# Performance work log

Measured on AMD Instinct MI355X. Metric: run time of the kernel, lower is better.

## Reference

```python
import jax, jax.numpy as jnp
import numpy as np

B, S, D, H, V = 4, 2048, 128, 4, 64
HD = D // H
ITERS = 3
SCALE = 1.0 / float(np.sqrt(HD))
APO = 0.2
TRP = 0.15
FC = 1.61803
EPS = 1e-5


def ln(x, g, b):
    m = x.mean(-1, keepdims=True)
    v = ((x - m) ** 2).mean(-1, keepdims=True)
    return (x - m) / jnp.sqrt(v + EPS) * g + b


def setup_inputs() -> dict:
    key = jax.random.key(0)
    ks = iter(jax.random.split(key, 64))

    def w(shape, s=0.02):
        return jax.random.normal(next(ks), shape, jnp.float32) * s

    return {
        "x": jax.random.normal(next(ks), (B, S, D), jnp.float32),
        "space": jax.random.normal(next(ks), (B, S, D), jnp.float32),
        # attn_norm
        "g_attn": jnp.ones(D), "b_attn": jnp.zeros(D),
        # RecursiveScaledDotProductAttention
        "Wq": w((D, D)), "Wk": w((D, D)), "Wv": w((D, D)),
        "Wo": w((D, D)), "bo": jnp.zeros(D),
        "Wg": w((D, 2 * D)), "bg": jnp.zeros(D),
        "Wobs": w((H, D)), "bobs": jnp.zeros(H),
        # trp_norm + TraumaResolutionPathLayer
        "g_trp": jnp.ones(D), "b_trp": jnp.zeros(D),
        "Wt": w((V, D)), "bt": jnp.zeros(V),
        "Wc": w((V, D)), "bc": jnp.zeros(V),
        "Ws": w((V, D)), "bs": jnp.zeros(V),
        "Wr": w((V, 3 * V)), "br": jnp.zeros(V),
        "fv": jnp.ones(V) * FC,
        "Wop": w((D, V)), "bop": jnp.zeros(D),
        # MorphogenesisFFN
        "g_ffn": jnp.ones(D), "b_ffn": jnp.zeros(D),
        "W1": w((4 * D, D)), "b1": jnp.zeros(4 * D),
        "W2": w((D, 4 * D)), "b2": jnp.zeros(D),
        "Wsg": w((D, D)), "bsg": jnp.zeros(D),
        # ApophasisLayer
        "g_apo": jnp.ones(D), "b_apo": jnp.zeros(D),
        "Wn": w((D, D)), "bn": jnp.zeros(D),
    }


def reference(x, space, g_attn, b_attn, Wq, Wk, Wv, Wo, bo, Wg, bg, Wobs, bobs,
              g_trp, b_trp, Wt, bt, Wc, bc, Ws, bs, Wr, br, fv, Wop, bop,
              g_ffn, b_ffn, W1, b1, W2, b2, Wsg, bsg, g_apo, b_apo, Wn, bn):
    # --- recursive attention (autopoiesis loop, eval mode: dropout = identity) ---
    xn = ln(x, g_attn, b_attn)
    obs = xn.mean(1, keepdims=True)                      # [B,1,D] observer_state default
    infl = (obs @ Wobs.T + bobs).transpose(0, 2, 1)[..., None]  # [B,H,1,1] per-head bias
    cur = xn
    for _ in range(ITERS):
        q = (cur @ Wq.T).reshape(B, S, H, HD).transpose(0, 2, 1, 3)
        k = (cur @ Wk.T).reshape(B, S, H, HD).transpose(0, 2, 1, 3)
        v = (cur @ Wv.T).reshape(B, S, H, HD).transpose(0, 2, 1, 3)
        scores = jnp.einsum('bhqd,bhkd->bhqk', q, k) * SCALE + infl
        aw = jax.nn.softmax(scores, axis=-1)             # [B,H,S,S]
        ao = jnp.einsum('bhqk,bhkd->bhqd', aw, v).transpose(0, 2, 1, 3).reshape(B, S, D)
        out = ao @ Wo.T + bo
        gate = jax.nn.sigmoid(jnp.concatenate([cur, out], -1) @ Wg.T + bg)
        cur = cur * (1 - gate) + out * gate
    x = x + cur
    # --- Trauma Resolution Path ---
    xn2 = ln(x, g_trp, b_trp)
    tv = xn2 @ Wt.T + bt                                 # [B,S,V]
    cv = jnp.broadcast_to(xn2.mean(1, keepdims=True) @ Wc.T + bc, tv.shape)
    sv = space @ Ws.T + bs
    rgate = jax.nn.sigmoid(jnp.concatenate([tv, cv, sv], -1) @ Wr.T + br)
    cn = jnp.maximum(jnp.linalg.norm(cv, axis=-1, keepdims=True), 1e-8)
    sn = jnp.maximum(jnp.linalg.norm(sv, axis=-1, keepdims=True), 1e-8)
    align = (cv * sv).sum(-1, keepdims=True) / (cn * sn)
    resolved = tv + TRP * (-align * (fv - tv) * rgate)
    x = x + resolved @ Wop.T + bop
    # --- Morphogenesis FFN ---
    xn3 = ln(x, g_ffn, b_ffn)
    ff = jax.nn.gelu(xn3 @ W1.T + b1, approximate=False) @ W2.T + b2
    x = x + jax.nn.sigmoid(xn3 @ Wsg.T + bsg) * ff
    # --- Apophasis ---
    x = x - APO * jnp.tanh(ln(x, g_apo, b_apo) @ Wn.T + bn)
    return x, aw
```

## Files before the change

### kernel.cpp

```cpp
#include <hip/hip_runtime.h>
#include <cstdint>
#include <cstddef>


typedef unsigned short u16;
typedef __attribute__((ext_vector_type(8))) short short8;
typedef __attribute__((ext_vector_type(4))) float f32x4;
typedef __attribute__((ext_vector_type(2))) unsigned uint32x2;

#define B_ 4
#define S_ 2048
#define D_ 128
#define H_ 4
#define M_ 8192
#define SCALE2_ 0.25503472510324417f
#define APO_ 0.2f
#define TRP_ 0.15f
#define EPS_ 1e-5f

__device__ __forceinline__ float fexp2(float x){ return __builtin_amdgcn_exp2f(x); }

__device__ __forceinline__ u16 f2bf(float f){
  unsigned u = __float_as_uint(f);
  unsigned r = ((u >> 16) & 1u) + 0x7fffu;
  return (u16)((u + r) >> 16);
}
__device__ __forceinline__ float bf2f(u16 u){ return __uint_as_float(((unsigned)u) << 16); }
__device__ __forceinline__ float sigm(float x){ return 1.0f/(1.0f + __expf(-x)); }

__device__ __forceinline__ unsigned cvtpk_bf16(float lo, float hi){
  unsigned r;
  asm("v_cvt_pk_bf16_f32 %0, %1, %2" : "=v"(r) : "v"(lo), "v"(hi));
  return r;
}

#define LDS_BARRIER() __asm__ volatile("s_waitcnt lgkmcnt(0)\n\ts_barrier" ::: "memory")

struct WSrc { const float* s[13]; };
__global__ __launch_bounds__(256) void prep_k(WSrc w, u16* __restrict__ dst,
    const float* __restrict__ x_in, const float* __restrict__ g,
    const float* __restrict__ b, u16* __restrict__ cg0){
  if (blockIdx.x < 1168){
    int idx = blockIdx.x*256 + threadIdx.x;
    if (idx >= 299008) return;
    const int sz[13] = {16384,16384,16384,16384,32768,8192,8192,12288,8192,65536,65536,16384,16384};
    int off = idx;
    #pragma unroll
    for (int seg = 0; seg < 13; ++seg){
      if (off < sz[seg]) { dst[idx] = f2bf(w.s[seg][off]); return; }
      off -= sz[seg];
    }
  } else {
    int wv = threadIdx.x >> 6, lane = threadIdx.x & 63;
    int row = (blockIdx.x - 1168)*4 + wv;
    size_t rb = (size_t)row * D_;
    float v0 = x_in[rb + lane], v1 = x_in[rb + lane + 64];
    float s = v0 + v1;
    #pragma unroll
    for (int m = 1; m < 64; m <<= 1) s += __shfl_xor(s, m, 64);
    float mean = s * (1.0f/128.0f);
    float d0 = v0 - mean, d1 = v1 - mean;
    float vv = d0*d0 + d1*d1;
    #pragma unroll
    for (int m = 1; m < 64; m <<= 1) vv += __shfl_xor(vv, m, 64);
    float rstd = rsqrtf(vv * (1.0f/128.0f) + EPS_);
    cg0[rb + lane]      = f2bf(d0*rstd*g[lane]    + b[lane]);
    cg0[rb + lane + 64] = f2bf(d1*rstd*g[lane+64] + b[lane+64]);
  }
}

__global__ __launch_bounds__(512) void colmean_k(const u16* __restrict__ lnb,
    const float* __restrict__ Wc, const float* __restrict__ bc,
    float* __restrict__ cv, float* __restrict__ cn){
  __shared__ float red2[32][128];
  __shared__ float cmS[128];
  int b = blockIdx.x;
  int tid = threadIdx.x;
  int rg = tid >> 4, c8 = (tid & 15)*8;
  const u16* pp = lnb + (size_t)b*S_*D_ + (size_t)rg*D_ + c8;
  float acc[8];
  #pragma unroll
  for (int j = 0; j < 8; ++j) acc[j] = 0.f;
  #pragma unroll 4
  for (int i = 0; i < 64; ++i){
    short8 v = *(const short8*)(pp + (size_t)i*32*D_);
    #pragma unroll
    for (int j = 0; j < 8; ++j) acc[j] += bf2f((u16)v[j]);
  }
  #pragma unroll
  for (int j = 0; j < 8; ++j) red2[rg][c8 + j] = acc[j];
  __syncthreads();
  if (tid < 128){
    float s = 0.f;
    #pragma unroll
    for (int r = 0; r < 32; ++r) s += red2[r][tid];
    cmS[tid] = s * (1.0f/2048.0f);
  }
  __syncthreads();
  if (tid < 64){
    int n = tid;
    const float* wrow = Wc + n*D_;
    float sacc = bc[n];
    #pragma unroll 4
    for (int dd = 0; dd < D_; ++dd) sacc += cmS[dd]*wrow[dd];
    cv[b*64 + n] = sacc;
    float sq = sacc*sacc;
    #pragma unroll
    for (int m = 1; m < 64; m <<= 1) sq += __shfl_xor(sq, m, 64);
    if (n == 0) cn[b] = fmaxf(sqrtf(sq), 1e-8f);
  }
}

__global__ __launch_bounds__(256) void gemm_qkv(const u16* __restrict__ A,
    const u16* __restrict__ W, u16* __restrict__ qh, u16* __restrict__ kh, u16* __restrict__ vt){
  __shared__ u16 Asm[64*136];
  __shared__ u16 Bsm[64*136];
  const int m0 = blockIdx.x*64, n0 = blockIdx.y*64;
  int tid = threadIdx.x;
  int wv = tid >> 6, lane = tid & 63, quad = lane >> 4, l15 = lane & 15;
  int wm = wv >> 1, wn = wv & 1;
  {
    int sr = tid >> 2, cb = (tid & 3)*32;
    const u16* ag = A + (size_t)(m0 + sr)*128 + cb;
    const u16* bg = W + (size_t)(n0 + sr)*128 + cb;
    short8 a0 = *(const short8*)(ag + 0);
    short8 a1 = *(const short8*)(ag + 8);
    short8 a2 = *(const short8*)(ag + 16);
    short8 a3 = *(const short8*)(ag + 24);
    short8 b0 = *(const short8*)(bg + 0);
    short8 b1 = *(const short8*)(bg + 8);
    short8 b2 = *(const short8*)(bg + 16);
    short8 b3 = *(const short8*)(bg + 24);
    *(short8*)(Asm + sr*136 + cb + 0)  = a0;
    *(short8*)(Asm + sr*136 + cb + 8)  = a1;
    *(short8*)(Asm + sr*136 + cb + 16) = a2;
    *(short8*)(Asm + sr*136 + cb + 24) = a3;
    *(short8*)(Bsm + sr*136 + cb + 0)  = b0;
    *(short8*)(Bsm + sr*136 + cb + 8)  = b1;
    *(short8*)(Bsm + sr*136 + cb + 16) = b2;
    *(short8*)(Bsm + sr*136 + cb + 24) = b3;
  }
  LDS_BARRIER();
  f32x4 acc[2][2];
  #pragma unroll
  for (int i = 0; i < 2; ++i)
    #pragma unroll
    for (int j = 0; j < 2; ++j) acc[i][j] = (f32x4){0.f,0.f,0.f,0.f};
  #pragma unroll
  for (int k0 = 0; k0 < 128; k0 += 32){
    short8 af0 = *(const short8*)(Asm + (wm*32      + l15)*136 + k0 + quad*8);
    short8 af1 = *(const short8*)(Asm + (wm*32 + 16 + l15)*136 + k0 + quad*8);
    short8 bf0 = *(const short8*)(Bsm + (wn*32      + l15)*136 + k0 + quad*8);
    short8 bf1 = *(const short8*)(Bsm + (wn*32 + 16 + l15)*136 + k0 + quad*8);
    acc[0][0] = __builtin_amdgcn_mfma_f32_16x16x32_bf16(af0, bf0, acc[0][0], 0,0,0);
    acc[0][1] = __builtin_amdgcn_mfma_f32_16x16x32_bf16(af0, bf1, acc[0][1], 0,0,0);
    acc[1][0] = __builtin_amdgcn_mfma_f32_16x16x32_bf16(af1, bf0, acc[1][0], 0,0,0);
    acc[1][1] = __builtin_amdgcn_mfma_f32_16x16x32_bf16(af1, bf1, acc[1][1], 0,0,0);
  }
  #pragma unroll
  for (int ms = 0; ms < 2; ++ms)
    #pragma unroll
    for (int ns = 0; ns < 2; ++ns){
      int mb = m0 + wm*32 + ms*16 + quad*4;
      int nn = n0 + wn*32 + ns*16 + l15;
      int which = nn >> 7, col = nn & 127, h = col >> 5, hd = col & 31;
      f32x4 c = acc[ms][ns];
      #pragma unroll
      for (int r = 0; r < 4; ++r){
        int m = mb + r, b = m >> 11, s = m & 2047;
        if (which == 0)      qh[((size_t)(b*H_+h)*S_ + s)*32 + hd] = f2bf(c[r]);
        else if (which == 1) kh[((size_t)(b*H_+h)*S_ + s)*32 + hd] = f2bf(c[r]);
        else                 vt[((size_t)(b*H_+h)*32 + hd)*S_ + s] = f2bf(c[r]);
      }
    }
}

template<bool WRITE_AW>
__global__ __launch_bounds__(256) void attn_k(const u16* __restrict__ qh, const u16* __restrict__ kh,
    const u16* __restrict__ vT, u16* __restrict__ ao_bf, float* __restrict__ aw){
  __shared__ u16 Ks[2][128*40];
  __shared__ u16 Vs[2][32*136];
  __shared__ u16 Ps[4*16*136];
  int L = blockIdx.y*32 + blockIdx.x;
  int xcd = L & 7, j = L >> 3;
  int bh = 2*xcd + (j >> 5);
  int q0 = (j & 31)*64;
  int b = bh >> 2, h = bh & 3;
  int tid = threadIdx.x, wv = tid >> 6, lane = tid & 63, quad = lane >> 4, l15 = lane & 15;
  int qrow = q0 + wv*16 + l15;
  const size_t bhS = (size_t)bh * S_;
  short8 qf = *(const short8*)(qh + (bhS + qrow)*32 + quad*8);
  int krow = tid >> 1, kseg = (tid & 1)*16;
  const u16* kg = kh + (bhS + krow)*32 + kseg;
  int vrow = tid >> 3, vseg = (tid & 7)*16;
  const u16* vg = vT + ((size_t)bh*32 + vrow)*S_ + vseg;
  f32x4 zero = {0.f,0.f,0.f,0.f};
  f32x4 ao0 = zero, ao1 = zero;
  float lsum = 0.f, rinv = 1.0f, nls = 0.f;
  u16* PsW = Ps + wv*16*136;

  if constexpr (WRITE_AW){
    {
      short8 a0 = *(const short8*)(kg + 0);
      short8 a1 = *(const short8*)(kg + 8);
      *(short8*)(Ks[0] + krow*40 + kseg    ) = a0;
      *(short8*)(Ks[0] + krow*40 + kseg + 8) = a1;
    }
    #pragma unroll 2
    for (int t = 0; t < 16; ++t){
      LDS_BARRIER();
      short8 n0, n1;
      if (t < 15){
        n0 = *(const short8*)(kg + (size_t)(t+1)*4096 + 0);
        n1 = *(const short8*)(kg + (size_t)(t+1)*4096 + 8);
      }
      const u16* Kb = Ks[t & 1];
      #pragma unroll
      for (int jt = 0; jt < 8; ++jt){
        short8 kf = *(const short8*)(Kb + (jt*16 + l15)*40 + quad*8);
        f32x4 s = __builtin_amdgcn_mfma_f32_16x16x32_bf16(kf, qf, zero, 0,0,0);
        #pragma unroll
        for (int r = 0; r < 4; ++r) lsum += fexp2(s[r]*SCALE2_);
      }
      if (t < 15){
        u16* Kn = Ks[(t+1) & 1];
        *(short8*)(Kn + krow*40 + kseg    ) = n0;
        *(short8*)(Kn + krow*40 + kseg + 8) = n1;
      }
    }
    lsum += __shfl_xor(lsum, 16, 64);
    lsum += __shfl_xor(lsum, 32, 64);
    nls = -__log2f(lsum);
  }

  {
    short8 a0 = *(const short8*)(kg + 0);
    short8 a1 = *(const short8*)(kg + 8);
    short8 b0 = *(const short8*)(vg + 0);
    short8 b1 = *(const short8*)(vg + 8);
    *(short8*)(Ks[0] + krow*40 + kseg    ) = a0;
    *(short8*)(Ks[0] + krow*40 + kseg + 8) = a1;
    *(short8*)(Vs[0] + vrow*136 + vseg    ) = b0;
    *(short8*)(Vs[0] + vrow*136 + vseg + 8) = b1;
  }
  #pragma unroll 2
  for (int t = 0; t < 16; ++t){
    LDS_BARRIER();
    short8 kn0, kn1, vn0, vn1;
    if (t < 15){
      kn0 = *(const short8*)(kg + (size_t)(t+1)*4096 + 0);
      kn1 = *(const short8*)(kg + (size_t)(t+1)*4096 + 8);
      vn0 = *(const short8*)(vg + (size_t)(t+1)*128 + 0);
      vn1 = *(const short8*)(vg + (size_t)(t+1)*128 + 8);
    }
    const u16* Kb = Ks[t & 1];
    const u16* Vb = Vs[t & 1];
    int k0 = t*128;
    #pragma unroll
    for (int jt = 0; jt < 8; ++jt){
      short8 kf = *(const short8*)(Kb + (jt*16 + l15)*40 + quad*8);
      f32x4 s = __builtin_amdgcn_mfma_f32_16x16x32_bf16(kf, qf, zero, 0,0,0);
      float pv[4];
      #pragma unroll
      for (int r = 0; r < 4; ++r){
        float e;
        if constexpr (WRITE_AW) e = fexp2(__builtin_fmaf(s[r], SCALE2_, nls));
        else { e = fexp2(s[r]*SCALE2_); lsum += e; }
        pv[r] = e;
      }
      if constexpr (WRITE_AW){
        f32x4 st = {pv[0], pv[1], pv[2], pv[3]};
        *(f32x4*)(aw + (bhS + qrow)*S_ + k0 + jt*16 + quad*4) = st;
      }
      uint32x2 pk;
      pk[0] = cvtpk_bf16(pv[0], pv[1]);
      pk[1] = cvtpk_bf16(pv[2], pv[3]);
      *(uint32x2*)(PsW + l15*136 + jt*16 + quad*4) = pk;
    }
    __asm__ volatile("s_waitcnt lgkmcnt(0)" ::: "memory");
    #pragma unroll
    for (int jg = 0; jg < 4; ++jg){
      short8 pf  = *(const short8*)(PsW + l15*136 + jg*32 + quad*8);
      short8 vf0 = *(const short8*)(Vb + (l15     )*136 + jg*32 + quad*8);
      short8 vf1 = *(const short8*)(Vb + (16 + l15)*136 + jg*32 + quad*8);
      ao0 = __builtin_amdgcn_mfma_f32_16x16x32_bf16(vf0, pf, ao0, 0,0,0);
      ao1 = __builtin_amdgcn_mfma_f32_16x16x32_bf16(vf1, pf, ao1, 0,0,0);
    }
    if (t < 15){
      u16* Kn = Ks[(t+1) & 1];
      u16* Vn = Vs[(t+1) & 1];
      *(short8*)(Kn + krow*40 + kseg    ) = kn0;
      *(short8*)(Kn + krow*40 + kseg + 8) = kn1;
      *(short8*)(Vn + vrow*136 + vseg    ) = vn0;
      *(short8*)(Vn + vrow*136 + vseg + 8) = vn1;
    }
  }

  if constexpr (!WRITE_AW){
    lsum += __shfl_xor(lsum, 16, 64);
    lsum += __shfl_xor(lsum, 32, 64);
    rinv = 1.0f / lsum;
  }

  size_t rowbase = ((size_t)(b*S_ + qrow))*D_ + h*32;
  #pragma unroll
  for (int dt = 0; dt < 2; ++dt){
    f32x4 a = dt ? ao1 : ao0;
    uint32x2 pk;
    pk[0] = cvtpk_bf16(a[0]*rinv, a[1]*rinv);
    pk[1] = cvtpk_bf16(a[2]*rinv, a[3]*rinv);
    *(uint32x2*)(ao_bf + rowbase + dt*16 + quad*4) = pk;
  }
}

template<bool DO_QKV>
__global__ __launch_bounds__(256) void wqkv_k(const u16* __restrict__ cin,
    const u16* __restrict__ ao_bf, const u16* __restrict__ wo, const u16* __restrict__ wg,
    const u16* __restrict__ w3, const float* __restrict__ bo, const float* __restrict__ bg,
    u16* __restrict__ cout, u16* __restrict__ qh, u16* __restrict__ kh, u16* __restrict__ vt,
    const float* __restrict__ x_in, const float* __restrict__ g_trp,
    const float* __restrict__ b_trp, float* __restrict__ xbuf, u16* __restrict__ lnb){
  __shared__ u16 aoS[16*136];
  __shared__ u16 cuS[16*136];
  __shared__ u16 outS[16*136];
  __shared__ u16 coS[16*136];
  const int m0 = blockIdx.x*16;
  int tid = threadIdx.x, wv = tid >> 6, lane = tid & 63, quad = lane >> 4, l15 = lane & 15;
  {
    int row = tid >> 4, seg = (tid & 15)*8;
    *(short8*)(aoS + row*136 + seg) = *(const short8*)(ao_bf + (size_t)(m0+row)*128 + seg);
    *(short8*)(cuS + row*136 + seg) = *(const short8*)(cin   + (size_t)(m0+row)*128 + seg);
  }
  __syncthreads();
  f32x4 oacc[2] = {(f32x4){0,0,0,0},(f32x4){0,0,0,0}};
  #pragma unroll
  for (int kc = 0; kc < 4; ++kc){
    short8 af = *(const short8*)(aoS + l15*136 + kc*32 + quad*8);
    #pragma unroll
    for (int nt = 0; nt < 2; ++nt){
      int n = wv*32 + nt*16 + l15;
      short8 bfv = *(const short8*)(wo + (size_t)n*128 + kc*32 + quad*8);
      oacc[nt] = __builtin_amdgcn_mfma_f32_16x16x32_bf16(af, bfv, oacc[nt], 0,0,0);
    }
  }
  #pragma unroll
  for (int nt = 0; nt < 2; ++nt){
    int n = wv*32 + nt*16 + l15;
    float bias = bo[n];
    #pragma unroll
    for (int r = 0; r < 4; ++r){
      int m = quad*4 + r;
      outS[m*136 + n] = f2bf(oacc[nt][r] + bias);
    }
  }
  __syncthreads();
  f32x4 gacc[2] = {(f32x4){0,0,0,0},(f32x4){0,0,0,0}};
  #pragma unroll
  for (int kc = 0; kc < 8; ++kc){
    short8 af = (kc < 4) ? *(const short8*)(cuS  + l15*136 + kc*32 + quad*8)
                         : *(const short8*)(outS + l15*136 + (kc-4)*32 + quad*8);
    #pragma unroll
    for (int nt = 0; nt < 2; ++nt){
      int n = wv*32 + nt*16 + l15;
      short8 bfv = *(const short8*)(wg + (size_t)n*256 + kc*32 + quad*8);
      gacc[nt] = __builtin_amdgcn_mfma_f32_16x16x32_bf16(af, bfv, gacc[nt], 0,0,0);
    }
  }
  #pragma unroll
  for (int nt = 0; nt < 2; ++nt){
    int n = wv*32 + nt*16 + l15;
    float biasg = bg[n], biaso = bo[n];
    #pragma unroll
    for (int r = 0; r < 4; ++r){
      int m = quad*4 + r;
      float g = sigm(gacc[nt][r] + biasg);
      float c = bf2f(cuS[m*136 + n]);
      float o = oacc[nt][r] + biaso;
      u16 val = f2bf(c + g*(o - c));
      coS[m*136 + n] = val;
      if constexpr (DO_QKV) cout[(size_t)(m0+m)*128 + n] = val;
    }
  }
  __syncthreads();
  if constexpr (DO_QKV){
    f32x4 qacc[6];
    #pragma unroll
    for (int i = 0; i < 6; ++i) qacc[i] = (f32x4){0,0,0,0};
    #pragma unroll
    for (int kc = 0; kc < 4; ++kc){
      short8 af = *(const short8*)(coS + l15*136 + kc*32 + quad*8);
      #pragma unroll
      for (int nt = 0; nt < 6; ++nt){
        int n = wv*96 + nt*16 + l15;
        short8 bfv = *(const short8*)(w3 + (size_t)n*128 + kc*32 + quad*8);
        qacc[nt] = __builtin_amdgcn_mfma_f32_16x16x32_bf16(af, bfv, qacc[nt], 0,0,0);
      }
    }
    #pragma unroll
    for (int nt = 0; nt < 6; ++nt){
      int nn = wv*96 + nt*16 + l15;
      int which = nn >> 7, col = nn & 127, h = col >> 5, hd = col & 31;
      #pragma unroll
      for (int r = 0; r < 4; ++r){
        int m = m0 + quad*4 + r, b = m >> 11, s = m & 2047;
        if (which == 0)      qh[((size_t)(b*H_+h)*S_ + s)*32 + hd] = f2bf(qacc[nt][r]);
        else if (which == 1) kh[((size_t)(b*H_+h)*S_ + s)*32 + hd] = f2bf(qacc[nt][r]);
        else                 vt[((size_t)(b*H_+h)*32 + hd)*S_ + s] = f2bf(qacc[nt][r]);
      }
    }
  } else {
    for (int rr = wv*4; rr < wv*4 + 4; ++rr){
      size_t rb = (size_t)(m0+rr)*128;
      float v0 = x_in[rb + lane]      + bf2f(coS[rr*136 + lane]);
      float v1 = x_in[rb + lane + 64] + bf2f(coS[rr*136 + lane + 64]);
      xbuf[rb + lane] = v0; xbuf[rb + lane + 64] = v1;
      float s = v0 + v1;
      #pragma unroll
      for (int m = 1; m < 64; m <<= 1) s += __shfl_xor(s, m, 64);
      float mean = s * (1.0f/128.0f);
      float d0 = v0 - mean, d1 = v1 - mean;
      float vv = d0*d0 + d1*d1;
      #pragma unroll
      for (int m = 1; m < 64; m <<= 1) vv += __shfl_xor(vv, m, 64);
      float rstd = rsqrtf(vv * (1.0f/128.0f) + EPS_);
      lnb[rb + lane]      = f2bf(d0*rstd*g_trp[lane]    + b_trp[lane]);
      lnb[rb + lane + 64] = f2bf(d1*rstd*g_trp[lane+64] + b_trp[lane+64]);
    }
  }
}

__global__ __launch_bounds__(256) void uber_k(const u16* __restrict__ lnb,
    const float* __restrict__ space, const float* __restrict__ xbuf,
    const float* __restrict__ cv, const float* __restrict__ cn,
    const u16* __restrict__ wt, const float* __restrict__ bt,
    const u16* __restrict__ wsx, const float* __restrict__ bs,
    const u16* __restrict__ wr, const float* __restrict__ br, const float* __restrict__ fv,
    const u16* __restrict__ wop, const float* __restrict__ bop,
    const float* __restrict__ g_ffn, const float* __restrict__ b_ffn,
    const u16* __restrict__ w1, const float* __restrict__ b1,
    const u16* __restrict__ w2, const float* __restrict__ b2,
    const u16* __restrict__ wsg, const float* __restrict__ bsg,
    const float* __restrict__ g_apo, const float* __restrict__ b_apo,
    const u16* __restrict__ wn, const float* __restrict__ bn,
    float* __restrict__ out_x){
  __shared__ u16 xnS[16*136];
  __shared__ u16 spS[16*136];
  __shared__ u16 CcS[16*200];
  __shared__ float svF[16*64];
  __shared__ u16 RsS[16*72];
  __shared__ float xrF[16*128];
  __shared__ u16 midS[16*536];
  __shared__ float alignS[16];
  const int m0 = blockIdx.x*16;
  const int bidx = m0 >> 11;
  int tid = threadIdx.x, wv = tid >> 6, lane = tid & 63, quad = lane >> 4, l15 = lane & 15;

  {
    int row = tid >> 4, seg = (tid & 15)*8;
    *(short8*)(xnS + row*136 + seg) = *(const short8*)(lnb + (size_t)(m0+row)*128 + seg);
    const float* sp = space + (size_t)(m0+row)*128 + seg;
    short8 pk;
    #pragma unroll
    for (int i = 0; i < 8; ++i) pk[i] = (short)f2bf(sp[i]);
    *(short8*)(spS + row*136 + seg) = pk;
    f32x4 xa = *(const f32x4*)(xbuf + (size_t)(m0+row)*128 + seg);
    f32x4 xb = *(const f32x4*)(xbuf + (size_t)(m0+row)*128 + seg + 4);
    *(f32x4*)(xrF + row*128 + seg) = xa;
    *(f32x4*)(xrF + row*128 + seg + 4) = xb;
  }
  __syncthreads();

  f32x4 tvacc = {0,0,0,0};
  {
    int n = wv*16 + l15;
    #pragma unroll
    for (int kc = 0; kc < 4; ++kc){
      short8 af  = *(const short8*)(xnS + l15*136 + kc*32 + quad*8);
      short8 bfv = *(const short8*)(wt + (size_t)n*128 + kc*32 + quad*8);
      tvacc = __builtin_amdgcn_mfma_f32_16x16x32_bf16(af, bfv, tvacc, 0,0,0);
    }
    float bias = bt[n];
    #pragma unroll
    for (int r = 0; r < 4; ++r){
      tvacc[r] += bias;
      CcS[(quad*4 + r)*200 + n] = f2bf(tvacc[r]);
    }
  }
  {
    int n = wv*16 + l15;
    f32x4 sva = {0,0,0,0};
    #pragma unroll
    for (int kc = 0; kc < 4; ++kc){
      short8 af  = *(const short8*)(spS + l15*136 + kc*32 + quad*8);
      short8 bfv = *(const short8*)(wsx + (size_t)n*128 + kc*32 + quad*8);
      sva = __builtin_amdgcn_mfma_f32_16x16x32_bf16(af, bfv, sva, 0,0,0);
    }
    float bias = bs[n];
    #pragma unroll
    for (int r = 0; r < 4; ++r){
      float v = sva[r] + bias;
      int m = quad*4 + r;
      CcS[m*200 + 128 + n] = f2bf(v);
      svF[m*64 + n] = v;
    }
    int row = tid >> 4, c4 = (tid & 15)*4;
    #pragma unroll
    for (int i = 0; i < 4; ++i)
      CcS[row*200 + 64 + c4 + i] = f2bf(cv[bidx*64 + c4 + i]);
  }
  __syncthreads();

  {
    float cnb = cn[bidx];
    for (int rr = wv*4; rr < wv*4 + 4; ++rr){
      float s = svF[rr*64 + lane];
      float c = cv[bidx*64 + lane];
      float dot = c*s, ss = s*s;
      #pragma unroll
      for (int m = 1; m < 64; m <<= 1){ dot += __shfl_xor(dot, m, 64); ss += __shfl_xor(ss, m, 64); }
      if (lane == 0){
        float sn = fmaxf(sqrtf(ss), 1e-8f);
        alignS[rr] = dot / (cnb * sn);
      }
    }
  }
  __syncthreads();

  {
    int n = wv*16 + l15;
    f32x4 ra = {0,0,0,0};
    #pragma unroll
    for (int kc = 0; kc < 6; ++kc){
      short8 af  = *(const short8*)(CcS + l15*200 + kc*32 + quad*8);
      short8 bfv = *(const short8*)(wr + (size_t)n*192 + kc*32 + quad*8);
      ra = __builtin_amdgcn_mfma_f32_16x16x32_bf16(af, bfv, ra, 0,0,0);
    }
    float bias = br[n], fvn = fv[n];
    #pragma unroll
    for (int r = 0; r < 4; ++r){
      int m = quad*4 + r;
      float rg = sigm(ra[r] + bias);
      float t = tvacc[r];
      float res = t + TRP_*(-alignS[m]*(fvn - t)*rg);
      RsS[m*72 + n] = f2bf(res);
    }
  }
  __syncthreads();

  {
    f32x4 wa[2] = {(f32x4){0,0,0,0},(f32x4){0,0,0,0}};
    #pragma unroll
    for (int kc = 0; kc < 2; ++kc){
      short8 af = *(const short8*)(RsS + l15*72 + kc*32 + quad*8);
      #pragma unroll
      for (int nt = 0; nt < 2; ++nt){
        int n = wv*32 + nt*16 + l15;
        short8 bfv = *(const short8*)(wop + (size_t)n*64 + kc*32 + quad*8);
        wa[nt] = __builtin_amdgcn_mfma_f32_16x16x32_bf16(af, bfv, wa[nt], 0,0,0);
      }
    }
    #pragma unroll
    for (int nt = 0; nt < 2; ++nt){
      int n = wv*32 + nt*16 + l15;
      float bias = bop[n];
      #pragma unroll
      for (int r = 0; r < 4; ++r){
        int m = quad*4 + r;
        xrF[m*128 + n] += wa[nt][r] + bias;
      }
    }
  }
  __syncthreads();

  for (int rr = wv*4; rr < wv*4 + 4; ++rr){
    float v0 = xrF[rr*128 + lane], v1 = xrF[rr*128 + lane + 64];
    float s = v0 + v1;
    #pragma unroll
    for (int m = 1; m < 64; m <<= 1) s += __shfl_xor(s, m, 64);
    float mean = s * (1.0f/128.0f);
    float d0 = v0 - mean, d1 = v1 - mean;
    float vvv = d0*d0 + d1*d1;
    #pragma unroll
    for (int m = 1; m < 64; m <<= 1) vvv += __shfl_xor(vvv, m, 64);
    float rstd = rsqrtf(vvv * (1.0f/128.0f) + EPS_);
    xnS[rr*136 + lane]      = f2bf(d0*rstd*g_ffn[lane]    + b_ffn[lane]);
    xnS[rr*136 + lane + 64] = f2bf(d1*rstd*g_ffn[lane+64] + b_ffn[lane+64]);
  }
  __syncthreads();

  {
    f32x4 acc[8];
    #pragma unroll
    for (int i = 0; i < 8; ++i) acc[i] = (f32x4){0,0,0,0};
    #pragma unroll
    for (int kc = 0; kc < 4; ++kc){
      short8 af = *(const short8*)(xnS + l15*136 + kc*32 + quad*8);
      #pragma unroll
      for (int nt = 0; nt < 8; ++nt){
        int n = wv*128 + nt*16 + l15;
        short8 bfv = *(const short8*)(w1 + (size_t)n*128 + kc*32 + quad*8);
        acc[nt] = __builtin_amdgcn_mfma_f32_16x16x32_bf16(af, bfv, acc[nt], 0,0,0);
      }
    }
    #pragma unroll
    for (int nt = 0; nt < 8; ++nt){
      int n = wv*128 + nt*16 + l15;
      float bias = b1[n];
      #pragma unroll
      for (int r = 0; r < 4; ++r){
        int m = quad*4 + r;
        float lin = acc[nt][r] + bias;
        float ge = 0.5f*lin*(1.0f + erff(lin*0.70710678118654752f));
        midS[m*536 + n] = f2bf(ge);
      }
    }
  }
  __syncthreads();

  {
    f32x4 ffa[2] = {(f32x4){0,0,0,0},(f32x4){0,0,0,0}};
    #pragma unroll
    for (int kc = 0; kc < 16; ++kc){
      short8 af = *(const short8*)(midS + l15*536 + kc*32 + quad*8);
      #pragma unroll
      for (int nt = 0; nt < 2; ++nt){
        int n = wv*32 + nt*16 + l15;
        short8 bfv = *(const short8*)(w2 + (size_t)n*512 + kc*32 + quad*8);
        ffa[nt] = __builtin_amdgcn_mfma_f32_16x16x32_bf16(af, bfv, ffa[nt], 0,0,0);
      }
    }
    f32x4 sga[2] = {(f32x4){0,0,0,0},(f32x4){0,0,0,0}};
    #pragma unroll
    for (int kc = 0; kc < 4; ++kc){
      short8 af = *(const short8*)(xnS + l15*136 + kc*32 + quad*8);
      #pragma unroll
      for (int nt = 0; nt < 2; ++nt){
        int n = wv*32 + nt*16 + l15;
        short8 bfv = *(const short8*)(wsg + (size_t)n*128 + kc*32 + quad*8);
        sga[nt] = __builtin_amdgcn_mfma_f32_16x16x32_bf16(af, bfv, sga[nt], 0,0,0);
      }
    }
    #pragma unroll
    for (int nt = 0; nt < 2; ++nt){
      int n = wv*32 + nt*16 + l15;
      float b2n = b2[n], bsgn = bsg[n];
      #pragma unroll
      for (int r = 0; r < 4; ++r){
        int m = quad*4 + r;
        float ff = ffa[nt][r] + b2n;
        float sg = sigm(sga[nt][r] + bsgn);
        xrF[m*128 + n] += sg*ff;
      }
    }
  }
  __syncthreads();

  for (int rr = wv*4; rr < wv*4 + 4; ++rr){
    float v0 = xrF[rr*128 + lane], v1 = xrF[rr*128 + lane + 64];
    float s = v0 + v1;
    #pragma unroll
    for (int m = 1; m < 64; m <<= 1) s += __shfl_xor(s, m, 64);
    float mean = s * (1.0f/128.0f);
    float d0 = v0 - mean, d1 = v1 - mean;
    float vvv = d0*d0 + d1*d1;
    #pragma unroll
    for (int m = 1; m < 64; m <<= 1) vvv += __shfl_xor(vvv, m, 64);
    float rstd = rsqrtf(vvv * (1.0f/128.0f) + EPS_);
    xnS[rr*136 + lane]      = f2bf(d0*rstd*g_apo[lane]    + b_apo[lane]);
    xnS[rr*136 + lane + 64] = f2bf(d1*rstd*g_apo[lane+64] + b_apo[lane+64]);
  }
  __syncthreads();

  {
    f32x4 na[2] = {(f32x4){0,0,0,0},(f32x4){0,0,0,0}};
    #pragma unroll
    for (int kc = 0; kc < 4; ++kc){
      short8 af = *(const short8*)(xnS + l15*136 + kc*32 + quad*8);
      #pragma unroll
      for (int nt = 0; nt < 2; ++nt){
        int n = wv*32 + nt*16 + l15;
        short8 bfv = *(const short8*)(wn + (size_t)n*128 + kc*32 + quad*8);
        na[nt] = __builtin_amdgcn_mfma_f32_16x16x32_bf16(af, bfv, na[nt], 0,0,0);
      }
    }
    #pragma unroll
    for (int nt = 0; nt < 2; ++nt){
      int n = wv*32 + nt*16 + l15;
      float bias = bn[n];
      #pragma unroll
      for (int r = 0; r < 4; ++r){
        int m = quad*4 + r;
        out_x[(size_t)(m0+m)*128 + n] = xrF[m*128 + n] - APO_*tanhf(na[nt][r] + bias);
      }
    }
  }
}

extern "C" void kernel_launch(void* const* d_in, const int* in_sizes, int n_in,
                              void* d_out, int out_size, void* d_ws, size_t ws_size,
                              hipStream_t stream){
  (void)in_sizes; (void)n_in; (void)out_size; (void)ws_size;
  const float* x_in   = (const float*)d_in[0];
  const float* space  = (const float*)d_in[1];
  const float* g_attn = (const float*)d_in[2];
  const float* b_attn = (const float*)d_in[3];
  const float* Wq     = (const float*)d_in[4];
  const float* Wk     = (const float*)d_in[5];
  const float* Wv     = (const float*)d_in[6];
  const float* Wo     = (const float*)d_in[7];
  const float* bo     = (const float*)d_in[8];
  const float* Wg     = (const float*)d_in[9];
  const float* bg     = (const float*)d_in[10];
  const float* g_trp  = (const float*)d_in[13];
  const float* b_trp  = (const float*)d_in[14];
  const float* Wt     = (const float*)d_in[15];
  const float* bt     = (const float*)d_in[16];
  const float* Wc     = (const float*)d_in[17];
  const float* bc     = (const float*)d_in[18];
  const float* Ws_    = (const float*)d_in[19];
  const float* bs     = (const float*)d_in[20];
  const float* Wr     = (const float*)d_in[21];
  const float* br     = (const float*)d_in[22];
  const float* fv     = (const float*)d_in[23];
  const float* Wop    = (const float*)d_in[24];
  const float* bop    = (const float*)d_in[25];
  const float* g_ffn  = (const float*)d_in[26];
  const float* b_ffn  = (const float*)d_in[27];
  const float* W1_    = (const float*)d_in[28];
  const float* b1     = (const float*)d_in[29];
  const float* W2_    = (const float*)d_in[30];
  const float* b2     = (const float*)d_in[31];
  const float* Wsg_   = (const float*)d_in[32];
  const float* bsg    = (const float*)d_in[33];
  const float* g_apo  = (const float*)d_in[34];
  const float* b_apo  = (const float*)d_in[35];
  const float* Wn_    = (const float*)d_in[36];
  const float* bn     = (const float*)d_in[37];

  char* base = (char*)d_ws;
  size_t off = 0;
  auto alloc = [&](size_t bytes)->char* {
    char* r = base + off; off += (bytes + 255) & ~(size_t)255; return r; };
  u16*  wbf   = (u16*) alloc((size_t)299008*2);
  u16*  cg0   = (u16*) alloc((size_t)M_*D_*2);
  u16*  cg1   = (u16*) alloc((size_t)M_*D_*2);
  u16*  qh    = (u16*) alloc((size_t)16*S_*32*2);
  u16*  kh    = (u16*) alloc((size_t)16*S_*32*2);
  u16*  vt    = (u16*) alloc((size_t)16*32*S_*2);
  u16*  ao_bf = (u16*) alloc((size_t)M_*D_*2);
  u16*  lnb   = (u16*) alloc((size_t)M_*D_*2);
  float* xbuf = (float*)alloc((size_t)M_*D_*4);
  float* cvb  = (float*)alloc(4*64*4);
  float* cnb  = (float*)alloc(4*4);

  u16* wqkv = wbf;
  u16* wo   = wbf + 49152;
  u16* wg   = wbf + 65536;
  u16* wt   = wbf + 98304;
  u16* wsx  = wbf + 106496;
  u16* wr   = wbf + 114688;
  u16* wop  = wbf + 126976;
  u16* w1   = wbf + 135168;
  u16* w2   = wbf + 200704;
  u16* wsgp = wbf + 266240;
  u16* wn   = wbf + 282624;

  float* out_x = (float*)d_out;
  float* aw    = out_x + (size_t)M_*D_;

  WSrc wsrc;
  wsrc.s[0]=Wq; wsrc.s[1]=Wk; wsrc.s[2]=Wv; wsrc.s[3]=Wo; wsrc.s[4]=Wg;
  wsrc.s[5]=Wt; wsrc.s[6]=Ws_; wsrc.s[7]=Wr; wsrc.s[8]=Wop; wsrc.s[9]=W1_;
  wsrc.s[10]=W2_; wsrc.s[11]=Wsg_; wsrc.s[12]=Wn_;

  prep_k<<<1168 + M_/4, 256, 0, stream>>>(wsrc, wbf, x_in, g_attn, b_attn, cg0);
  gemm_qkv<<<dim3(M_/64, 6), 256, 0, stream>>>(cg0, wqkv, qh, kh, vt);

  attn_k<false><<<dim3(S_/64, 16), 256, 0, stream>>>(qh, kh, vt, ao_bf, nullptr);
  wqkv_k<true ><<<M_/16, 256, 0, stream>>>(cg0, ao_bf, wo, wg, wqkv, bo, bg, cg1, qh, kh, vt,
                                           x_in, g_trp, b_trp, xbuf, lnb);
  attn_k<false><<<dim3(S_/64, 16), 256, 0, stream>>>(qh, kh, vt, ao_bf, nullptr);
  wqkv_k<true ><<<M_/16, 256, 0, stream>>>(cg1, ao_bf, wo, wg, wqkv, bo, bg, cg0, qh, kh, vt,
                                           x_in, g_trp, b_trp, xbuf, lnb);
  attn_k<true ><<<dim3(S_/64, 16), 256, 0, stream>>>(qh, kh, vt, ao_bf, aw);
  wqkv_k<false><<<M_/16, 256, 0, stream>>>(cg0, ao_bf, wo, wg, wqkv, bo, bg, cg1, qh, kh, vt,
                                           x_in, g_trp, b_trp, xbuf, lnb);

  colmean_k<<<4, 512, 0, stream>>>(lnb, Wc, bc, cvb, cnb);

  uber_k<<<M_/16, 256, 0, stream>>>(lnb, space, xbuf, cvb, cnb,
      wt, bt, wsx, bs, wr, br, fv, wop, bop,
      g_ffn, b_ffn, w1, b1, w2, b2, wsgp, bsg,
      g_apo, b_apo, wn, bn, out_x);
}
```

Baseline: 214.1 us.

## Fuse column-mean into LN epilogue via atomics and compute cv in uber kernel

Removes the separate colmean_k launch. Per-batch column sums of the trp-normalized activations are now accumulated with atomicAdd in the final wqkv_k epilogue, into a buffer zeroed in prep_k. Each uber_k block then recomputes the 64-wide cv projection and its norm from those sums. This saves a small serial 4-block kernel and a full re-read of lnb, but adds atomics and redundant per-block matvecs. An LDS barrier was also added in attn_k, apparently to protect the shared K buffer when it is reused between passes.

```diff
diff --git a/kernel.cpp b/kernel.cpp
--- a/kernel.cpp
+++ b/kernel.cpp
@@ -39,8 +39,9 @@
 struct WSrc { const float* s[13]; };
 __global__ __launch_bounds__(256) void prep_k(WSrc w, u16* __restrict__ dst,
     const float* __restrict__ x_in, const float* __restrict__ g,
-    const float* __restrict__ b, u16* __restrict__ cg0){
+    const float* __restrict__ b, u16* __restrict__ cg0, float* __restrict__ colsum){
   if (blockIdx.x < 1168){
+    if (blockIdx.x == 0 && threadIdx.x < 512) colsum[threadIdx.x] = 0.f;
     int idx = blockIdx.x*256 + threadIdx.x;
     if (idx >= 299008) return;
     const int sz[13] = {16384,16384,16384,16384,32768,8192,8192,12288,8192,65536,65536,16384,16384};
@@ -66,48 +67,6 @@
     float rstd = rsqrtf(vv * (1.0f/128.0f) + EPS_);
     cg0[rb + lane]      = f2bf(d0*rstd*g[lane]    + b[lane]);
     cg0[rb + lane + 64] = f2bf(d1*rstd*g[lane+64] + b[lane+64]);
-  }
-}
-
-__global__ __launch_bounds__(512) void colmean_k(const u16* __restrict__ lnb,
-    const float* __restrict__ Wc, const float* __restrict__ bc,
-    float* __restrict__ cv, float* __restrict__ cn){
-  __shared__ float red2[32][128];
-  __shared__ float cmS[128];
-  int b = blockIdx.x;
-  int tid = threadIdx.x;
-  int rg = tid >> 4, c8 = (tid & 15)*8;
-  const u16* pp = lnb + (size_t)b*S_*D_ + (size_t)rg*D_ + c8;
-  float acc[8];
-  #pragma unroll
-  for (int j = 0; j < 8; ++j) acc[j] = 0.f;
-  #pragma unroll 4
-  for (int i = 0; i < 64; ++i){
-    short8 v = *(const short8*)(pp + (size_t)i*32*D_);
-    #pragma unroll
-    for (int j = 0; j < 8; ++j) acc[j] += bf2f((u16)v[j]);
-  }
-  #pragma unroll
-  for (int j = 0; j < 8; ++j) red2[rg][c8 + j] = acc[j];
-  __syncthreads();
-  if (tid < 128){
-    float s = 0.f;
-    #pragma unroll
-    for (int r = 0; r < 32; ++r) s += red2[r][tid];
-    cmS[tid] = s * (1.0f/2048.0f);
-  }
-  __syncthreads();
-  if (tid < 64){
-    int n = tid;
-    const float* wrow = Wc + n*D_;
-    float sacc = bc[n];
-    #pragma unroll 4
-    for (int dd = 0; dd < D_; ++dd) sacc += cmS[dd]*wrow[dd];
-    cv[b*64 + n] = sacc;
-    float sq = sacc*sacc;
-    #pragma unroll
-    for (int m = 1; m < 64; m <<= 1) sq += __shfl_xor(sq, m, 64);
-    if (n == 0) cn[b] = fmaxf(sqrtf(sq), 1e-8f);
   }
 }
 
@@ -231,6 +190,7 @@
     lsum += __shfl_xor(lsum, 16, 64);
     lsum += __shfl_xor(lsum, 32, 64);
     nls = -__log2f(lsum);
+    LDS_BARRIER();
   }
 
   {
@@ -319,7 +279,8 @@
     const u16* __restrict__ w3, const float* __restrict__ bo, const float* __restrict__ bg,
     u16* __restrict__ cout, u16* __restrict__ qh, u16* __restrict__ kh, u16* __restrict__ vt,
     const float* __restrict__ x_in, const float* __restrict__ g_trp,
-    const float* __restrict__ b_trp, float* __restrict__ xbuf, u16* __restrict__ lnb){
+    const float* __restrict__ b_trp, float* __restrict__ xbuf, u16* __restrict__ lnb,
+    float* __restrict__ colsum){
   __shared__ u16 aoS[16*136];
   __shared__ u16 cuS[16*136];
   __shared__ u16 outS[16*136];
@@ -409,6 +370,8 @@
       }
     }
   } else {
+    const int bidx = m0 >> 11;
+    float cs0 = 0.f, cs1 = 0.f;
     for (int rr = wv*4; rr < wv*4 + 4; ++rr){
       size_t rb = (size_t)(m0+rr)*128;
       float v0 = x_in[rb + lane]      + bf2f(coS[rr*136 + lane]);
@@ -423,15 +386,27 @@
       #pragma unroll
       for (int m = 1; m < 64; m <<= 1) vv += __shfl_xor(vv, m, 64);
       float rstd = rsqrtf(vv * (1.0f/128.0f) + EPS_);
-      lnb[rb + lane]      = f2bf(d0*rstd*g_trp[lane]    + b_trp[lane]);
-      lnb[rb + lane + 64] = f2bf(d1*rstd*g_trp[lane+64] + b_trp[lane+64]);
+      u16 l0v = f2bf(d0*rstd*g_trp[lane]    + b_trp[lane]);
+      u16 l1v = f2bf(d1*rstd*g_trp[lane+64] + b_trp[lane+64]);
+      lnb[rb + lane]      = l0v;
+      lnb[rb + lane + 64] = l1v;
+      cs0 += bf2f(l0v);
+      cs1 += bf2f(l1v);
+    }
+    float* red = (float*)outS;
+    red[wv*128 + lane]      = cs0;
+    red[wv*128 + lane + 64] = cs1;
+    __syncthreads();
+    if (tid < 128){
+      float s = red[tid] + red[128 + tid] + red[256 + tid] + red[384 + tid];
+      atomicAdd(&colsum[bidx*128 + tid], s);
     }
   }
 }
 
 __global__ __launch_bounds__(256) void uber_k(const u16* __restrict__ lnb,
     const float* __restrict__ space, const float* __restrict__ xbuf,
-    const float* __restrict__ cv, const float* __restrict__ cn,
+    const float* __restrict__ colsum, const float* __restrict__ Wc, const float* __restrict__ bc,
     const u16* __restrict__ wt, const float* __restrict__ bt,
     const u16* __restrict__ wsx, const float* __restrict__ bs,
     const u16* __restrict__ wr, const float* __restrict__ br, const float* __restrict__ fv,
@@ -451,6 +426,8 @@
   __shared__ float xrF[16*128];
   __shared__ u16 midS[16*536];
   __shared__ float alignS[16];
+  __shared__ float cvS[64];
+  __shared__ float cnS;
   const int m0 = blockIdx.x*16;
   const int bidx = m0 >> 11;
   int tid = threadIdx.x, wv = tid >> 6, lane = tid & 63, quad = lane >> 4, l15 = lane & 15;
@@ -468,6 +445,18 @@
     *(f32x4*)(xrF + row*128 + seg) = xa;
     *(f32x4*)(xrF + row*128 + seg + 4) = xb;
   }
+  if (tid < 64){
+    const float* wrow = Wc + tid*128;
+    const float* cb = colsum + bidx*128;
+    float sacc = bc[tid];
+    #pragma unroll 4
+    for (int dd = 0; dd < 128; ++dd) sacc += (cb[dd]*(1.0f/2048.0f))*wrow[dd];
+    cvS[tid] = sacc;
+    float sq = sacc*sacc;
+    #pragma unroll
+    for (int m = 1; m < 64; m <<= 1) sq += __shfl_xor(sq, m, 64);
+    if (tid == 0) cnS = fmaxf(sqrtf(sq), 1e-8f);
+  }
   __syncthreads();
 
   f32x4 tvacc = {0,0,0,0};
@@ -506,15 +495,15 @@
     int row = tid >> 4, c4 = (tid & 15)*4;
     #pragma unroll
     for (int i = 0; i < 4; ++i)
-      CcS[row*200 + 64 + c4 + i] = f2bf(cv[bidx*64 + c4 + i]);
-  }
-  __syncthreads();
-
-  {
-    float cnb = cn[bidx];
+      CcS[row*200 + 64 + c4 + i] = f2bf(cvS[c4 + i]);
+  }
+  __syncthreads();
+
+  {
+    float cnb = cnS;
     for (int rr = wv*4; rr < wv*4 + 4; ++rr){
       float s = svF[rr*64 + lane];
-      float c = cv[bidx*64 + lane];
+      float c = cvS[lane];
       float dot = c*s, ss = s*s;
       #pragma unroll
       for (int m = 1; m < 64; m <<= 1){ dot += __shfl_xor(dot, m, 64); ss += __shfl_xor(ss, m, 64); }
@@ -750,8 +739,7 @@
   u16*  ao_bf = (u16*) alloc((size_t)M_*D_*2);
   u16*  lnb   = (u16*) alloc((size_t)M_*D_*2);
   float* xbuf = (float*)alloc((size_t)M_*D_*4);
-  float* cvb  = (float*)alloc(4*64*4);
-  float* cnb  = (float*)alloc(4*4);
+  float* colsum = (float*)alloc(4*128*4);
 
   u16* wqkv = wbf;
   u16* wo   = wbf + 49152;
@@ -773,22 +761,20 @@
   wsrc.s[5]=Wt; wsrc.s[6]=Ws_; wsrc.s[7]=Wr; wsrc.s[8]=Wop; wsrc.s[9]=W1_;
   wsrc.s[10]=W2_; wsrc.s[11]=Wsg_; wsrc.s[12]=Wn_;
 
-  prep_k<<<1168 + M_/4, 256, 0, stream>>>(wsrc, wbf, x_in, g_attn, b_attn, cg0);
+  prep_k<<<1168 + M_/4, 256, 0, stream>>>(wsrc, wbf, x_in, g_attn, b_attn, cg0, colsum);
   gemm_qkv<<<dim3(M_/64, 6), 256, 0, stream>>>(cg0, wqkv, qh, kh, vt);
 
   attn_k<false><<<dim3(S_/64, 16), 256, 0, stream>>>(qh, kh, vt, ao_bf, nullptr);
   wqkv_k<true ><<<M_/16, 256, 0, stream>>>(cg0, ao_bf, wo, wg, wqkv, bo, bg, cg1, qh, kh, vt,
-                                           x_in, g_trp, b_trp, xbuf, lnb);
+                                           x_in, g_trp, b_trp, xbuf, lnb, colsum);
   attn_k<false><<<dim3(S_/64, 16), 256, 0, stream>>>(qh, kh, vt, ao_bf, nullptr);
   wqkv_k<true ><<<M_/16, 256, 0, stream>>>(cg1, ao_bf, wo, wg, wqkv, bo, bg, cg0, qh, kh, vt,
-                                           x_in, g_trp, b_trp, xbuf, lnb);
+                                           x_in, g_trp, b_trp, xbuf, lnb, colsum);
   attn_k<true ><<<dim3(S_/64, 16), 256, 0, stream>>>(qh, kh, vt, ao_bf, aw);
   wqkv_k<false><<<M_/16, 256, 0, stream>>>(cg0, ao_bf, wo, wg, wqkv, bo, bg, cg1, qh, kh, vt,
-                                           x_in, g_trp, b_trp, xbuf, lnb);
-
-  colmean_k<<<4, 512, 0, stream>>>(lnb, Wc, bc, cvb, cnb);
-
-  uber_k<<<M_/16, 256, 0, stream>>>(lnb, space, xbuf, cvb, cnb,
+                                           x_in, g_trp, b_trp, xbuf, lnb, colsum);
+
+  uber_k<<<M_/16, 256, 0, stream>>>(lnb, space, xbuf, colsum, Wc, bc,
       wt, bt, wsx, bs, wr, br, fv, wop, bop,
       g_ffn, b_ffn, w1, b1, w2, b2, wsgp, bsg,
       g_apo, b_apo, wn, bn, out_x);
```

After: 207.1 us (median of 2 runs). 3.3% less time.
